# Kernel optimization log

Hardware: AMD Instinct MI355X
Metric: run time of the kernel (lower is better)

The kernel has to match this reference:

```python
import jax, jax.numpy as jnp
import numpy as np

N_FEAT = 9
D_MODEL = 128
N_HEADS = 4
LN_EPS = 1e-5


def setup_inputs() -> dict:
    key = jax.random.key(0)
    ks = jax.random.split(key, 16)
    d, F = D_MODEL, N_FEAT
    s = 0.02
    return {
        "x": jax.random.normal(ks[0], (8, 256, 16, F), dtype=jnp.float32),
        # per-band Linear(1, d): weight (F, d), bias (F, d)
        "band_W": jax.random.normal(ks[1], (F, d), dtype=jnp.float32) * s,
        "band_b": jax.random.normal(ks[2], (F, d), dtype=jnp.float32) * s,
        "freq_pos": jax.random.normal(ks[3], (1, F, d), dtype=jnp.float32) * s,
        # MultiheadAttention packed in-proj (3d, d) and out-proj (d, d)
        "in_proj_w": jax.random.normal(ks[4], (3 * d, d), dtype=jnp.float32) * s,
        "in_proj_b": jax.random.normal(ks[5], (3 * d,), dtype=jnp.float32) * s,
        "out_proj_w": jax.random.normal(ks[6], (d, d), dtype=jnp.float32) * s,
        "out_proj_b": jax.random.normal(ks[7], (d,), dtype=jnp.float32) * s,
        # gate: Linear(F*d, d)
        "gate_w": jax.random.normal(ks[8], (d, F * d), dtype=jnp.float32) * s,
        "gate_b": jax.random.normal(ks[9], (d,), dtype=jnp.float32) * s,
        # output_proj: Linear(F*d, 2d) -> GELU -> Linear(2d, d) -> LayerNorm(d)
        "proj1_w": jax.random.normal(ks[10], (2 * d, F * d), dtype=jnp.float32) * s,
        "proj1_b": jax.random.normal(ks[11], (2 * d,), dtype=jnp.float32) * s,
        "proj2_w": jax.random.normal(ks[12], (d, 2 * d), dtype=jnp.float32) * s,
        "proj2_b": jax.random.normal(ks[13], (d,), dtype=jnp.float32) * s,
        "ln_g": jnp.ones((d,), dtype=jnp.float32),
        "ln_b": jnp.zeros((d,), dtype=jnp.float32),
    }


def _forward(x, band_W, band_b, freq_pos, in_proj_w, in_proj_b,
             out_proj_w, out_proj_b, gate_w, gate_b,
             proj1_w, proj1_b, proj2_w, proj2_b, ln_g, ln_b):
    B, T, C, F = x.shape
    d, H = D_MODEL, N_HEADS
    dh = d // H
    N = B * T * C
    xf = x.reshape(N, F)
    # per-band Linear(1, d) + positional embedding -> (N, F, d)
    tok = xf[:, :, None] * band_W[None] + band_b[None] + freq_pos
    # packed QKV projection (torch MHA semantics)
    qkv = jnp.einsum('nfd,ed->nfe', tok, in_proj_w) + in_proj_b
    q, k, v = jnp.split(qkv, 3, axis=-1)
    q = q.reshape(N, F, H, dh)
    k = k.reshape(N, F, H, dh)
    v = v.reshape(N, F, H, dh)
    scores = jnp.einsum('nqhd,nkhd->nhqk', q, k) / jnp.sqrt(jnp.float32(dh))
    attn = jax.nn.softmax(scores, axis=-1)
    ctx = jnp.einsum('nhqk,nkhd->nqhd', attn, v).reshape(N, F, d)
    attn_out = ctx @ out_proj_w.T + out_proj_b
    flat = attn_out.reshape(N, F * d)
    gate = jax.nn.sigmoid(flat @ gate_w.T + gate_b)
    h = jax.nn.gelu(flat @ proj1_w.T + proj1_b, approximate=False)
    y = h @ proj2_w.T + proj2_b
    mu = jnp.mean(y, axis=-1, keepdims=True)
    var = jnp.mean(jnp.square(y - mu), axis=-1, keepdims=True)
    y = (y - mu) * jax.lax.rsqrt(var + LN_EPS) * ln_g + ln_b
    out = y * gate
    return out.reshape(B, T, C, d)


def reference(x, band_W, band_b, freq_pos, in_proj_w, in_proj_b,
              out_proj_w, out_proj_b, gate_w, gate_b,
              proj1_w, proj1_b, proj2_w, proj2_b, ln_g, ln_b):
    return _forward(x, band_W, band_b, freq_pos, in_proj_w, in_proj_b,
                    out_proj_w, out_proj_b, gate_w, gate_b,
                    proj1_w, proj1_b, proj2_w, proj2_b, ln_g, ln_b)
```

## Files before the change

### kernel.cpp

```cpp
#include <hip/hip_runtime.h>

namespace {
constexpr int FB = 9;
constexpr int FD = 1152;
constexpr float LN_EPS = 1e-5f;
constexpr int NT = 512;

typedef __attribute__((ext_vector_type(8))) short short8v;
typedef __attribute__((ext_vector_type(4))) float float4v;

constexpr int WSA_F  = 0;
constexpr int WSC_F  = 3456;
constexpr int COEF_F = 6912;
constexpr int BF_F   = 8352;
constexpr int OPA_F  = 8736;
constexpr int P2F_B  = 71808;
constexpr int WTA_B  = 137344;

constexpr int LDS_BYTES = 51200;
constexpr int L_GATE = 43008;
constexpr int L_COEF = 43008;
constexpr int L_SX   = 48768;

constexpr int NB_WTA  = 72;
constexpr int NB_BIAS = 384;
constexpr int NB_P2   = 64;

__device__ __forceinline__ unsigned short f2bf(float f) {
    unsigned u = __builtin_bit_cast(unsigned, f);
    u += 0x7FFFu + ((u >> 16) & 1u);
    return (unsigned short)(u >> 16);
}
__device__ __forceinline__ unsigned pkr(float lo, float hi) {
    const unsigned a = __builtin_bit_cast(unsigned, lo) + 0x8000u;
    const unsigned b = __builtin_bit_cast(unsigned, hi) + 0x8000u;
    return __builtin_amdgcn_perm(b, a, 0x07060302u);
}
#define MFMA16x32(a, b, c) __builtin_amdgcn_mfma_f32_16x16x32_bf16(a, b, c, 0, 0, 0)
}

__global__ void precompAC(const float* __restrict__ bW, const float* __restrict__ bb,
                          const float* __restrict__ fp, const float* __restrict__ ipw,
                          const float* __restrict__ ipb, float* __restrict__ ws)
{
    __shared__ float sw[128], sc[128];
    const int f = blockIdx.x, t = threadIdx.x;
    if (t < 128) { sw[t] = bW[f * 128 + t]; sc[t] = bb[f * 128 + t] + fp[f * 128 + t]; }
    __syncthreads();
    const float* row = ipw + (size_t)t * 128;
    float a = 0.f, c = 0.f;
    for (int k = 0; k < 128; k += 4) {
        const float4 w = *(const float4*)(row + k);
        a += sw[k]*w.x + sw[k+1]*w.y + sw[k+2]*w.z + sw[k+3]*w.w;
        c += sc[k]*w.x + sc[k+1]*w.y + sc[k+2]*w.z + sc[k+3]*w.w;
    }
    ws[WSA_F + f * 384 + t] = a;
    ws[WSC_F + f * 384 + t] = c + ipb[t];
}

__global__ void precompScoreOPA(const float* __restrict__ ws, const float* __restrict__ opw,
                                float* __restrict__ wso)
{
    const int b = blockIdx.x, t = threadIdx.x;
    if (b == 0) {
        if (t >= 324) return;
        const int h = t / 81, r = t % 81, fq = r / 9, fk = r % 9;
        const float* A = ws + WSA_F;
        const float* C = ws + WSC_F;
        const float* aq = A + fq * 384 + h * 32;
        const float* ak = A + fk * 384 + 128 + h * 32;
        const float* cq = C + fq * 384 + h * 32;
        const float* ck = C + fk * 384 + 128 + h * 32;
        float s2 = 0.f, s1q = 0.f, s1k = 0.f, s0 = 0.f;
        #pragma unroll
        for (int d = 0; d < 32; ++d) {
            s2  += aq[d] * ak[d];
            s1q += aq[d] * ck[d];
            s1k += cq[d] * ak[d];
            s0  += cq[d] * ck[d];
        }
        const float sc = 0.17677669529663687f;
        float* row = wso + COEF_F + (h * 9 + fq) * 40;
        row[fk]      = s2  * sc;
        row[10 + fk] = s1q * sc;
        row[20 + fk] = s1k * sc;
        row[30 + fk] = s0  * sc;
    } else {
        const int id = (b - 1) * 512 + t;
        if (id >= 9216) return;
        const int row = id >> 7, j = id & 127;
        const int h = row / 18, kk = row - h * 18;
        const float* av = (kk < 9) ? (ws + WSA_F + kk * 384 + 256)
                                   : (ws + WSC_F + (kk - 9) * 384 + 256);
        const float* op = opw + (size_t)j * 128 + h * 32;
        const float* avh = av + h * 32;
        float s = 0.f;
        #pragma unroll
        for (int ii = 0; ii < 32; ++ii) s += op[ii] * avh[ii];
        wso[OPA_F + row * 128 + j] = s;
    }
}

__global__ __launch_bounds__(512)
void precompWBP(const float* __restrict__ gw, const float* __restrict__ gb,
                const float* __restrict__ p1w, const float* __restrict__ p1b,
                const float* __restrict__ opb, const float* __restrict__ p2w,
                const float* __restrict__ wsf,
                unsigned short* __restrict__ wta, unsigned short* __restrict__ p2f,
                float* __restrict__ ws)
{
    __shared__ float smem[128 * 73 + 128 * 49];
    const int bid = blockIdx.x, t = threadIdx.x;
    if (bid < NB_WTA) {
        float* s_opaT = smem;
        float* s_winT = smem + 128 * 73;
        const int fq = bid % 9, oct = bid / 9;
        const int e0 = oct * 48;
        for (int i = t; i < 9216; i += 512) {
            const int r = i >> 7, j = i & 127;
            s_opaT[j * 73 + r] = wsf[OPA_F + i];
        }
        for (int i = t; i < 6144; i += 512) {
            const int el = i >> 7, j = i & 127;
            const int e = e0 + el;
            const float* Win = (e < 128) ? gw + (size_t)e * FD : p1w + (size_t)(e - 128) * FD;
            s_winT[j * 49 + el] = Win[fq * 128 + j];
        }
        __syncthreads();
        for (int d = t; d < 3456; d += 512) {
            const int el = d / 72, r = d - el * 72;
            const int e = e0 + el;
            float acc = 0.f;
            #pragma unroll 8
            for (int j = 0; j < 128; ++j)
                acc += s_winT[j * 49 + el] * s_opaT[j * 73 + r];
            const int h = r / 18, kk = r - h * 18;
            const int K = (h * 9 + fq) * 18 + kk;
            const int ks = K >> 5, slot = K & 31;
            const int lane = (e & 15) + 16 * (slot >> 3);
            wta[((size_t)((e >> 4) * 21 + ks) * 64 + lane) * 8 + (slot & 7)] = f2bf(acc);
        }
        if (fq == 0) {
            for (int d = t; d < 48 * 24; d += 512) {
                const int el = d / 24, Kp = 648 + d % 24;
                const int e = e0 + el;
                const int ks = Kp >> 5, slot = Kp & 31;
                const int lane = (e & 15) + 16 * (slot >> 3);
                wta[((size_t)((e >> 4) * 21 + ks) * 64 + lane) * 8 + (slot & 7)] = 0;
            }
        }
    } else if (bid < NB_WTA + NB_BIAS) {
        const int e = bid - NB_WTA;
        const float* Win = (e < 128) ? gw + (size_t)e * FD : p1w + (size_t)(e - 128) * FD;
        float acc = 0.f;
        for (int m = t; m < FD; m += 512) acc += Win[m] * opb[m & 127];
        #pragma unroll
        for (int off = 32; off > 0; off >>= 1) acc += __shfl_xor(acc, off);
        const int lane = t & 63, wid = t >> 6;
        if (lane == 0) smem[wid] = acc;
        __syncthreads();
        if (t == 0) {
            float s = (e < 128) ? gb[e] : p1b[e - 128];
            #pragma unroll
            for (int w = 0; w < 8; ++w) s += smem[w];
            ws[BF_F + e] = s;
        }
    } else {
        const int id = (bid - NB_WTA - NB_BIAS) * 512 + t;
        const int j = id & 7, lane = (id >> 3) & 63, ks = (id >> 9) & 7, nt = id >> 12;
        const int i = nt * 16 + (lane & 15);
        const int r = ks * 32 + (lane >> 4) * 8 + j;
        p2f[id] = f2bf(p2w[i * 256 + r]);
    }
}

__global__ __launch_bounds__(NT, 4)
void fba_main(const float* __restrict__ x, const float* __restrict__ p2b,
              const float* __restrict__ lng, const float* __restrict__ lnb,
              const float* __restrict__ wsf,
              const unsigned short* __restrict__ p2frag,
              const unsigned short* __restrict__ wta,
              float* __restrict__ out)
{
    __shared__ float4 lds4[LDS_BYTES / 16];
    char* lds = (char*)lds4;
    unsigned short* hfrag = (unsigned short*)lds;
    unsigned short* gateb = (unsigned short*)(lds + L_GATE);
    float* scoef = (float*)(lds + L_COEF);
    float* sx    = (float*)(lds + L_SX);

    const int t = threadIdx.x, lane = t & 63, wid = t >> 6;
    const int col = lane & 15, rg = lane >> 4;
    const int n0 = blockIdx.x * 32;

    for (int i = t; i < 1440; i += NT) scoef[i] = wsf[COEF_F + i];
    for (int i = t; i < 288;  i += NT) sx[i] = x[(size_t)n0 * FB + i];
    if (t < 128) *(float4*)(lds + 40960 + t * 16) = float4{0.f, 0.f, 0.f, 0.f};
    __syncthreads();

    for (int id = t; id < 1152; id += NT) {
        const int p = id >> 5, g = id & 31;
        const int fq = p % 9;
        const float* cf = scoef + p * 40;
        const float* xg = sx + g * FB;
        const float xq = xg[fq];
        float sc[9];
        float m = -1e30f;
        #pragma unroll
        for (int fk = 0; fk < 9; ++fk) {
            const float xk = xg[fk];
            const float v = (cf[fk] * xk + cf[10 + fk]) * xq + cf[20 + fk] * xk + cf[30 + fk];
            sc[fk] = v;
            m = fmaxf(m, v);
        }
        float sum = 0.f;
        #pragma unroll
        for (int fk = 0; fk < 9; ++fk) { sc[fk] = __expf(sc[fk] - m); sum += sc[fk]; }
        const float inv = 1.f / sum;
        float v[18];
        #pragma unroll
        for (int fk = 0; fk < 9; ++fk) {
            const float a = sc[fk] * inv;
            v[fk]     = a * xg[fk];
            v[9 + fk] = a;
        }
        const int mg = g >> 4, gl = g & 15;
        const int K0 = p * 18;
        #pragma unroll
        for (int qq = 0; qq < 9; ++qq) {
            const int K = K0 + 2 * qq;
            const int ks = K >> 5, slot = K & 31;
            const int row = ks * 2 + mg;
            const int u = gl + 16 * (slot >> 3);
            *(unsigned*)(lds + row * 1024 + u * 16 + (slot & 7) * 2) = pkr(v[2 * qq], v[2 * qq + 1]);
        }
    }
    __syncthreads();

    const int ng = wid;
    float4v acc0[3], acc1[3];
    #pragma unroll
    for (int q = 0; q < 3; ++q) {
        const float b = wsf[BF_F + (ng * 3 + q) * 16 + col];
        acc0[q] = float4v{b, b, b, b};
        acc1[q] = float4v{b, b, b, b};
    }
    const unsigned short* bbase = wta + (size_t)(ng * 3) * 21 * 512 + lane * 8;
    #define BLOAD(ks, q) (*(const short8v*)(bbase + ((size_t)(q) * 21 + (ks)) * 512))
    short8v cur0 = BLOAD(0, 0), cur1 = BLOAD(0, 1), cur2 = BLOAD(0, 2);
    #pragma unroll 4
    for (int ks = 0; ks < 20; ++ks) {
        const short8v nxt0 = BLOAD(ks + 1, 0);
        const short8v nxt1 = BLOAD(ks + 1, 1);
        const short8v nxt2 = BLOAD(ks + 1, 2);
        const short8v a0 = *(const short8v*)(lds + ((ks * 2 + 0) * 64 + lane) * 16);
        const short8v a1 = *(const short8v*)(lds + ((ks * 2 + 1) * 64 + lane) * 16);
        acc0[0] = MFMA16x32(a0, cur0, acc0[0]);
        acc1[0] = MFMA16x32(a1, cur0, acc1[0]);
        acc0[1] = MFMA16x32(a0, cur1, acc0[1]);
        acc1[1] = MFMA16x32(a1, cur1, acc1[1]);
        acc0[2] = MFMA16x32(a0, cur2, acc0[2]);
        acc1[2] = MFMA16x32(a1, cur2, acc1[2]);
        cur0 = nxt0; cur1 = nxt1; cur2 = nxt2;
    }
    {
        const short8v a0 = *(const short8v*)(lds + ((20 * 2 + 0) * 64 + lane) * 16);
        const short8v a1 = *(const short8v*)(lds + ((20 * 2 + 1) * 64 + lane) * 16);
        acc0[0] = MFMA16x32(a0, cur0, acc0[0]);
        acc1[0] = MFMA16x32(a1, cur0, acc1[0]);
        acc0[1] = MFMA16x32(a0, cur1, acc0[1]);
        acc1[1] = MFMA16x32(a1, cur1, acc1[1]);
        acc0[2] = MFMA16x32(a0, cur2, acc0[2]);
        acc1[2] = MFMA16x32(a1, cur2, acc1[2]);
    }
    #undef BLOAD
    __syncthreads();

    #pragma unroll
    for (int q = 0; q < 3; ++q) {
        const int e = (ng * 3 + q) * 16 + col;
        #pragma unroll
        for (int j = 0; j < 4; ++j) {
            #pragma unroll
            for (int mi = 0; mi < 2; ++mi) {
                const float vv = (mi == 0) ? acc0[q][j] : acc1[q][j];
                const int token = mi * 16 + rg * 4 + j;
                if (e < 128) {
                    const float gv = 1.f / (1.f + __expf(-vv));
                    gateb[token * 128 + e] = (unsigned short)(gv * 65535.f + 0.5f);
                } else {
                    const int rr = e - 128;
                    const float hv = 0.5f * vv * (1.f + erff(vv * 0.70710678118654752f));
                    hfrag[mi * 4096 + (rr >> 5) * 512 + (rg * 4 + j + 16 * ((rr >> 3) & 3)) * 8 + (rr & 7)] = f2bf(hv);
                }
            }
        }
    }
    __syncthreads();

    if (wid < 2) {
        const int mm = wid;
        float4v y[8];
        float lg[8], lb[8];
        #pragma unroll
        for (int nt = 0; nt < 8; ++nt) {
            const int i = nt * 16 + col;
            const float b = p2b[i];
            y[nt] = float4v{b, b, b, b};
            lg[nt] = lng[i];
            lb[nt] = lnb[i];
        }
        for (int ks = 0; ks < 8; ++ks) {
            const short8v ah = *(const short8v*)(hfrag + mm * 4096 + ks * 512 + lane * 8);
            #pragma unroll
            for (int nt = 0; nt < 8; ++nt) {
                const short8v bw = *(const short8v*)(p2frag + ((nt * 8 + ks) * 64 + lane) * 8);
                y[nt] = MFMA16x32(ah, bw, y[nt]);
            }
        }
        #pragma unroll
        for (int j = 0; j < 4; ++j) {
            const int token = mm * 16 + rg * 4 + j;
            float s = 0.f;
            #pragma unroll
            for (int nt = 0; nt < 8; ++nt) s += y[nt][j];
            s += __shfl_xor(s, 1); s += __shfl_xor(s, 2);
            s += __shfl_xor(s, 4); s += __shfl_xor(s, 8);
            const float mu = s * (1.f / 128.f);
            float v2 = 0.f;
            #pragma unroll
            for (int nt = 0; nt < 8; ++nt) { const float dd = y[nt][j] - mu; v2 += dd * dd; }
            v2 += __shfl_xor(v2, 1); v2 += __shfl_xor(v2, 2);
            v2 += __shfl_xor(v2, 4); v2 += __shfl_xor(v2, 8);
            const float inv = rsqrtf(v2 * (1.f / 128.f) + LN_EPS);
            float* op = out + (size_t)(n0 + token) * 128;
            #pragma unroll
            for (int nt = 0; nt < 8; ++nt) {
                const int i = nt * 16 + col;
                const float gv = (float)gateb[token * 128 + i] * (1.f / 65535.f);
                op[i] = ((y[nt][j] - mu) * inv * lg[nt] + lb[nt]) * gv;
            }
        }
    }
}

extern "C" void kernel_launch(void* const* d_in, const int* in_sizes, int n_in,
                              void* d_out, int out_size, void* d_ws, size_t ws_size,
                              hipStream_t stream)
{
    const float* x          = (const float*)d_in[0];
    const float* band_W     = (const float*)d_in[1];
    const float* band_b     = (const float*)d_in[2];
    const float* freq_pos   = (const float*)d_in[3];
    const float* in_proj_w  = (const float*)d_in[4];
    const float* in_proj_b  = (const float*)d_in[5];
    const float* out_proj_w = (const float*)d_in[6];
    const float* out_proj_b = (const float*)d_in[7];
    const float* gate_w     = (const float*)d_in[8];
    const float* gate_b     = (const float*)d_in[9];
    const float* proj1_w    = (const float*)d_in[10];
    const float* proj1_b    = (const float*)d_in[11];
    const float* proj2_w    = (const float*)d_in[12];
    const float* proj2_b    = (const float*)d_in[13];
    const float* ln_g       = (const float*)d_in[14];
    const float* ln_b       = (const float*)d_in[15];
    float* outp = (float*)d_out;

    float* wsf = (float*)d_ws;
    unsigned short* p2f = (unsigned short*)((char*)d_ws + P2F_B);
    unsigned short* wta = (unsigned short*)((char*)d_ws + WTA_B);

    const int Ntok = in_sizes[0] / FB;
    const int nblk = Ntok / 32;

    hipLaunchKernelGGL(precompAC,       dim3(9),   dim3(384), 0, stream, band_W, band_b, freq_pos, in_proj_w, in_proj_b, wsf);
    hipLaunchKernelGGL(precompScoreOPA, dim3(19),  dim3(512), 0, stream, wsf, out_proj_w, wsf);
    hipLaunchKernelGGL(precompWBP,      dim3(NB_WTA + NB_BIAS + NB_P2), dim3(512), 0, stream,
                       gate_w, gate_b, proj1_w, proj1_b, out_proj_b, proj2_w, wsf, wta, p2f, wsf);
    hipLaunchKernelGGL(fba_main,        dim3(nblk), dim3(NT), 0, stream,
                       x, proj2_b, ln_g, ln_b, wsf, p2f, wta, outp);
}
```

Before: 79.16 us.

## Process 64 tokens per block with K-chunked A-build and split LayerNorm epilogue

Doubles the tokens per block from 32 to 64, so each wave reuses every loaded weight B-fragment across four M-tiles instead of two, halving global weight traffic per token. To fit LDS, the attention-derived A matrix is built and consumed in two K-chunks with a triple-buffered B prefetch. The final proj2+LayerNorm stage now uses all 8 waves, split across token tiles and column halves, with partial sums combined through LDS and a single-pass variance formula. This trades higher LDS usage (64KB), more accumulators per thread and extra barriers, which may reduce occupancy, for less weight reloading.

```diff
diff --git a/kernel.cpp b/kernel.cpp
--- a/kernel.cpp
+++ b/kernel.cpp
@@ -17,10 +17,11 @@
 constexpr int P2F_B  = 71808;
 constexpr int WTA_B  = 137344;
 
-constexpr int LDS_BYTES = 51200;
-constexpr int L_GATE = 43008;
-constexpr int L_COEF = 43008;
-constexpr int L_SX   = 48768;
+constexpr int LDS_BYTES = 65536;
+constexpr int L_GATE = 49152;
+constexpr int L_COEF = 49152;
+constexpr int L_SX   = 54912;
+constexpr int L_LNP  = 32768;
 
 constexpr int NB_WTA  = 72;
 constexpr int NB_BIAS = 384;
@@ -37,6 +38,35 @@
     return __builtin_amdgcn_perm(b, a, 0x07060302u);
 }
 #define MFMA16x32(a, b, c) __builtin_amdgcn_mfma_f32_16x16x32_bf16(a, b, c, 0, 0, 0)
+
+template<int KS0, int NKS>
+__device__ __forceinline__ void kchunk(const char* __restrict__ abase,
+                                       const unsigned short* __restrict__ bbase,
+                                       float4v (&acc)[3][4])
+{
+    short8v bq[3][3];
+    #pragma unroll
+    for (int q = 0; q < 3; ++q)
+        bq[0][q] = *(const short8v*)(bbase + ((size_t)q * 21 + KS0) * 512);
+    #pragma unroll
+    for (int q = 0; q < 3; ++q)
+        bq[1][q] = *(const short8v*)(bbase + ((size_t)q * 21 + KS0 + 1) * 512);
+    #pragma unroll
+    for (int kl = 0; kl < NKS; ++kl) {
+        if (kl + 2 < NKS) {
+            #pragma unroll
+            for (int q = 0; q < 3; ++q)
+                bq[(kl + 2) % 3][q] = *(const short8v*)(bbase + ((size_t)q * 21 + KS0 + kl + 2) * 512);
+        }
+        #pragma unroll
+        for (int m = 0; m < 4; ++m) {
+            const short8v a = *(const short8v*)(abase + kl * 4096 + m * 1024);
+            #pragma unroll
+            for (int q = 0; q < 3; ++q)
+                acc[q][m] = MFMA16x32(a, bq[kl % 3][q], acc[q][m]);
+        }
+    }
+}
 }
 
 __global__ void precompAC(const float* __restrict__ bW, const float* __restrict__ bb,
@@ -185,160 +215,151 @@
     __shared__ float4 lds4[LDS_BYTES / 16];
     char* lds = (char*)lds4;
     unsigned short* hfrag = (unsigned short*)lds;
+    float* lnp  = (float*)(lds + L_LNP);
     unsigned short* gateb = (unsigned short*)(lds + L_GATE);
     float* scoef = (float*)(lds + L_COEF);
     float* sx    = (float*)(lds + L_SX);
 
     const int t = threadIdx.x, lane = t & 63, wid = t >> 6;
     const int col = lane & 15, rg = lane >> 4;
-    const int n0 = blockIdx.x * 32;
+    const int n0 = blockIdx.x * 64;
 
     for (int i = t; i < 1440; i += NT) scoef[i] = wsf[COEF_F + i];
-    for (int i = t; i < 288;  i += NT) sx[i] = x[(size_t)n0 * FB + i];
-    if (t < 128) *(float4*)(lds + 40960 + t * 16) = float4{0.f, 0.f, 0.f, 0.f};
+    for (int i = t; i < 576;  i += NT) sx[i] = x[(size_t)n0 * FB + i];
+    if (t < 256) *(float4*)(lds + 11 * 4096 + t * 16) = float4{0.f, 0.f, 0.f, 0.f};
     __syncthreads();
 
-    for (int id = t; id < 1152; id += NT) {
-        const int p = id >> 5, g = id & 31;
-        const int fq = p % 9;
-        const float* cf = scoef + p * 40;
-        const float* xg = sx + g * FB;
-        const float xq = xg[fq];
-        float sc[9];
-        float m = -1e30f;
-        #pragma unroll
-        for (int fk = 0; fk < 9; ++fk) {
-            const float xk = xg[fk];
-            const float v = (cf[fk] * xk + cf[10 + fk]) * xq + cf[20 + fk] * xk + cf[30 + fk];
-            sc[fk] = v;
-            m = fmaxf(m, v);
-        }
-        float sum = 0.f;
-        #pragma unroll
-        for (int fk = 0; fk < 9; ++fk) { sc[fk] = __expf(sc[fk] - m); sum += sc[fk]; }
-        const float inv = 1.f / sum;
-        float v[18];
-        #pragma unroll
-        for (int fk = 0; fk < 9; ++fk) {
-            const float a = sc[fk] * inv;
-            v[fk]     = a * xg[fk];
-            v[9 + fk] = a;
-        }
-        const int mg = g >> 4, gl = g & 15;
-        const int K0 = p * 18;
-        #pragma unroll
-        for (int qq = 0; qq < 9; ++qq) {
-            const int K = K0 + 2 * qq;
-            const int ks = K >> 5, slot = K & 31;
-            const int row = ks * 2 + mg;
-            const int u = gl + 16 * (slot >> 3);
-            *(unsigned*)(lds + row * 1024 + u * 16 + (slot & 7) * 2) = pkr(v[2 * qq], v[2 * qq + 1]);
-        }
-    }
-    __syncthreads();
-
     const int ng = wid;
-    float4v acc0[3], acc1[3];
+    float4v acc[3][4];
     #pragma unroll
     for (int q = 0; q < 3; ++q) {
         const float b = wsf[BF_F + (ng * 3 + q) * 16 + col];
-        acc0[q] = float4v{b, b, b, b};
-        acc1[q] = float4v{b, b, b, b};
-    }
+        #pragma unroll
+        for (int m = 0; m < 4; ++m) acc[q][m] = float4v{b, b, b, b};
+    }
+    const char* abase = lds + lane * 16;
     const unsigned short* bbase = wta + (size_t)(ng * 3) * 21 * 512 + lane * 8;
-    #define BLOAD(ks, q) (*(const short8v*)(bbase + ((size_t)(q) * 21 + (ks)) * 512))
-    short8v cur0 = BLOAD(0, 0), cur1 = BLOAD(0, 1), cur2 = BLOAD(0, 2);
-    #pragma unroll 4
-    for (int ks = 0; ks < 20; ++ks) {
-        const short8v nxt0 = BLOAD(ks + 1, 0);
-        const short8v nxt1 = BLOAD(ks + 1, 1);
-        const short8v nxt2 = BLOAD(ks + 1, 2);
-        const short8v a0 = *(const short8v*)(lds + ((ks * 2 + 0) * 64 + lane) * 16);
-        const short8v a1 = *(const short8v*)(lds + ((ks * 2 + 1) * 64 + lane) * 16);
-        acc0[0] = MFMA16x32(a0, cur0, acc0[0]);
-        acc1[0] = MFMA16x32(a1, cur0, acc1[0]);
-        acc0[1] = MFMA16x32(a0, cur1, acc0[1]);
-        acc1[1] = MFMA16x32(a1, cur1, acc1[1]);
-        acc0[2] = MFMA16x32(a0, cur2, acc0[2]);
-        acc1[2] = MFMA16x32(a1, cur2, acc1[2]);
-        cur0 = nxt0; cur1 = nxt1; cur2 = nxt2;
-    }
-    {
-        const short8v a0 = *(const short8v*)(lds + ((20 * 2 + 0) * 64 + lane) * 16);
-        const short8v a1 = *(const short8v*)(lds + ((20 * 2 + 1) * 64 + lane) * 16);
-        acc0[0] = MFMA16x32(a0, cur0, acc0[0]);
-        acc1[0] = MFMA16x32(a1, cur0, acc1[0]);
-        acc0[1] = MFMA16x32(a0, cur1, acc0[1]);
-        acc1[1] = MFMA16x32(a1, cur1, acc1[1]);
-        acc0[2] = MFMA16x32(a0, cur2, acc0[2]);
-        acc1[2] = MFMA16x32(a1, cur2, acc1[2]);
-    }
-    #undef BLOAD
-    __syncthreads();
+
+    #pragma unroll 1
+    for (int chunk = 0; chunk < 2; ++chunk) {
+        const int p0 = (chunk == 0) ? 0 : 16;
+        const int np = (chunk == 0) ? 16 : 20;
+        const int ksbase = (chunk == 0) ? 0 : 9;
+        for (int id = t; id < np * 64; id += NT) {
+            const int p = p0 + (id >> 6), g = id & 63;
+            const int fq = p % 9;
+            const float* cf = scoef + p * 40;
+            const float* xg = sx + g * FB;
+            const float xq = xg[fq];
+            float sc[9];
+            float m = -1e30f;
+            #pragma unroll
+            for (int fk = 0; fk < 9; ++fk) {
+                const float xk = xg[fk];
+                const float v = (cf[fk] * xk + cf[10 + fk]) * xq + cf[20 + fk] * xk + cf[30 + fk];
+                sc[fk] = v;
+                m = fmaxf(m, v);
+            }
+            float sum = 0.f;
+            #pragma unroll
+            for (int fk = 0; fk < 9; ++fk) { sc[fk] = __expf(sc[fk] - m); sum += sc[fk]; }
+            const float inv = 1.f / sum;
+            float v[18];
+            #pragma unroll
+            for (int fk = 0; fk < 9; ++fk) {
+                const float a = sc[fk] * inv;
+                v[fk]     = a * xg[fk];
+                v[9 + fk] = a;
+            }
+            const int mg = g >> 4, gl = g & 15;
+            const int K0 = p * 18;
+            #pragma unroll
+            for (int qq = 0; qq < 9; ++qq) {
+                const int K = K0 + 2 * qq;
+                const int row = (K >> 5) - ksbase;
+                const int slot = K & 31;
+                const int u = gl + 16 * (slot >> 3);
+                *(unsigned*)(lds + row * 4096 + mg * 1024 + u * 16 + (slot & 7) * 2) = pkr(v[2 * qq], v[2 * qq + 1]);
+            }
+        }
+        __syncthreads();
+        if (chunk == 0) kchunk<0, 9>(abase, bbase, acc);
+        else            kchunk<9, 12>(abase, bbase, acc);
+        __syncthreads();
+    }
 
     #pragma unroll
     for (int q = 0; q < 3; ++q) {
         const int e = (ng * 3 + q) * 16 + col;
         #pragma unroll
-        for (int j = 0; j < 4; ++j) {
-            #pragma unroll
-            for (int mi = 0; mi < 2; ++mi) {
-                const float vv = (mi == 0) ? acc0[q][j] : acc1[q][j];
-                const int token = mi * 16 + rg * 4 + j;
+        for (int m = 0; m < 4; ++m) {
+            #pragma unroll
+            for (int j = 0; j < 4; ++j) {
+                const float vv = acc[q][m][j];
+                const int token = m * 16 + rg * 4 + j;
                 if (e < 128) {
                     const float gv = 1.f / (1.f + __expf(-vv));
                     gateb[token * 128 + e] = (unsigned short)(gv * 65535.f + 0.5f);
                 } else {
                     const int rr = e - 128;
                     const float hv = 0.5f * vv * (1.f + erff(vv * 0.70710678118654752f));
-                    hfrag[mi * 4096 + (rr >> 5) * 512 + (rg * 4 + j + 16 * ((rr >> 3) & 3)) * 8 + (rr & 7)] = f2bf(hv);
+                    hfrag[m * 4096 + (rr >> 5) * 512 + (rg * 4 + j + 16 * ((rr >> 3) & 3)) * 8 + (rr & 7)] = f2bf(hv);
                 }
             }
         }
     }
     __syncthreads();
 
-    if (wid < 2) {
-        const int mm = wid;
-        float4v y[8];
-        float lg[8], lb[8];
-        #pragma unroll
-        for (int nt = 0; nt < 8; ++nt) {
-            const int i = nt * 16 + col;
+    {
+        const int pm = wid >> 1, half = wid & 1;
+        float4v y[4];
+        float lg[4], lb[4];
+        #pragma unroll
+        for (int nti = 0; nti < 4; ++nti) {
+            const int i = (half * 4 + nti) * 16 + col;
             const float b = p2b[i];
-            y[nt] = float4v{b, b, b, b};
-            lg[nt] = lng[i];
-            lb[nt] = lnb[i];
-        }
+            y[nti] = float4v{b, b, b, b};
+            lg[nti] = lng[i];
+            lb[nti] = lnb[i];
+        }
+        #pragma unroll
         for (int ks = 0; ks < 8; ++ks) {
-            const short8v ah = *(const short8v*)(hfrag + mm * 4096 + ks * 512 + lane * 8);
-            #pragma unroll
-            for (int nt = 0; nt < 8; ++nt) {
-                const short8v bw = *(const short8v*)(p2frag + ((nt * 8 + ks) * 64 + lane) * 8);
-                y[nt] = MFMA16x32(ah, bw, y[nt]);
+            const short8v ah = *(const short8v*)(hfrag + pm * 4096 + ks * 512 + lane * 8);
+            #pragma unroll
+            for (int nti = 0; nti < 4; ++nti) {
+                const short8v bw = *(const short8v*)(p2frag + (((half * 4 + nti) * 8 + ks) * 64 + lane) * 8);
+                y[nti] = MFMA16x32(ah, bw, y[nti]);
             }
         }
         #pragma unroll
         for (int j = 0; j < 4; ++j) {
-            const int token = mm * 16 + rg * 4 + j;
-            float s = 0.f;
-            #pragma unroll
-            for (int nt = 0; nt < 8; ++nt) s += y[nt][j];
-            s += __shfl_xor(s, 1); s += __shfl_xor(s, 2);
-            s += __shfl_xor(s, 4); s += __shfl_xor(s, 8);
+            const int token = pm * 16 + rg * 4 + j;
+            float s = y[0][j] + y[1][j] + y[2][j] + y[3][j];
+            float qq = y[0][j]*y[0][j] + y[1][j]*y[1][j] + y[2][j]*y[2][j] + y[3][j]*y[3][j];
+            s  += __shfl_xor(s, 1);  s  += __shfl_xor(s, 2);
+            s  += __shfl_xor(s, 4);  s  += __shfl_xor(s, 8);
+            qq += __shfl_xor(qq, 1); qq += __shfl_xor(qq, 2);
+            qq += __shfl_xor(qq, 4); qq += __shfl_xor(qq, 8);
+            if (col == 0) {
+                lnp[token * 4 + half * 2]     = s;
+                lnp[token * 4 + half * 2 + 1] = qq;
+            }
+        }
+        __syncthreads();
+        #pragma unroll
+        for (int j = 0; j < 4; ++j) {
+            const int token = pm * 16 + rg * 4 + j;
+            const float s  = lnp[token * 4]     + lnp[token * 4 + 2];
+            const float qq = lnp[token * 4 + 1] + lnp[token * 4 + 3];
             const float mu = s * (1.f / 128.f);
-            float v2 = 0.f;
-            #pragma unroll
-            for (int nt = 0; nt < 8; ++nt) { const float dd = y[nt][j] - mu; v2 += dd * dd; }
-            v2 += __shfl_xor(v2, 1); v2 += __shfl_xor(v2, 2);
-            v2 += __shfl_xor(v2, 4); v2 += __shfl_xor(v2, 8);
-            const float inv = rsqrtf(v2 * (1.f / 128.f) + LN_EPS);
+            const float var = qq * (1.f / 128.f) - mu * mu;
+            const float inv = rsqrtf(var + LN_EPS);
             float* op = out + (size_t)(n0 + token) * 128;
             #pragma unroll
-            for (int nt = 0; nt < 8; ++nt) {
-                const int i = nt * 16 + col;
+            for (int nti = 0; nti < 4; ++nti) {
+                const int i = (half * 4 + nti) * 16 + col;
                 const float gv = (float)gateb[token * 128 + i] * (1.f / 65535.f);
-                op[i] = ((y[nt][j] - mu) * inv * lg[nt] + lb[nt]) * gv;
+                op[i] = ((y[nti][j] - mu) * inv * lg[nti] + lb[nti]) * gv;
             }
         }
     }
@@ -371,7 +392,7 @@
     unsigned short* wta = (unsigned short*)((char*)d_ws + WTA_B);
 
     const int Ntok = in_sizes[0] / FB;
-    const int nblk = Ntok / 32;
+    const int nblk = Ntok / 64;
 
     hipLaunchKernelGGL(precompAC,       dim3(9),   dim3(384), 0, stream, band_W, band_b, freq_pos, in_proj_w, in_proj_b, wsf);
     hipLaunchKernelGGL(precompScoreOPA, dim3(19),  dim3(512), 0, stream, wsf, out_proj_w, wsf);
```

Result: slower. 105.9 us (+33.8%).

## Fuse score/OPA precompute into weight-prep kernel and deepen B-fragment prefetch

Applied to the files above, without the earlier changes.

Removes the separate precompScoreOPA launch. Each WTA block now recomputes the out-proj×V product in LDS from a transposed out_proj_w, and one extra block computes the score coefficients. In the main kernel the first three k-steps of B fragments are issued before the setup barrier, and the loop prefetches three steps ahead through a rotating register buffer. The cost is redundant OPA computation across 72 blocks, a larger LDS footprint in the precompute kernel, and higher register pressure in the main kernel.

```diff
diff --git a/kernel.cpp b/kernel.cpp
--- a/kernel.cpp
+++ b/kernel.cpp
@@ -13,7 +13,6 @@
 constexpr int WSC_F  = 3456;
 constexpr int COEF_F = 6912;
 constexpr int BF_F   = 8352;
-constexpr int OPA_F  = 8736;
 constexpr int P2F_B  = 71808;
 constexpr int WTA_B  = 137344;
 
@@ -58,73 +57,48 @@
     ws[WSC_F + f * 384 + t] = c + ipb[t];
 }
 
-__global__ void precompScoreOPA(const float* __restrict__ ws, const float* __restrict__ opw,
-                                float* __restrict__ wso)
+__global__ __launch_bounds__(512)
+void precompMega(const float* __restrict__ gw, const float* __restrict__ gb,
+                 const float* __restrict__ p1w, const float* __restrict__ p1b,
+                 const float* __restrict__ opw, const float* __restrict__ opb,
+                 const float* __restrict__ p2w, const float* __restrict__ wsf,
+                 unsigned short* __restrict__ wta, unsigned short* __restrict__ p2f,
+                 float* __restrict__ ws)
 {
-    const int b = blockIdx.x, t = threadIdx.x;
-    if (b == 0) {
-        if (t >= 324) return;
-        const int h = t / 81, r = t % 81, fq = r / 9, fk = r % 9;
-        const float* A = ws + WSA_F;
-        const float* C = ws + WSC_F;
-        const float* aq = A + fq * 384 + h * 32;
-        const float* ak = A + fk * 384 + 128 + h * 32;
-        const float* cq = C + fq * 384 + h * 32;
-        const float* ck = C + fk * 384 + 128 + h * 32;
-        float s2 = 0.f, s1q = 0.f, s1k = 0.f, s0 = 0.f;
-        #pragma unroll
-        for (int d = 0; d < 32; ++d) {
-            s2  += aq[d] * ak[d];
-            s1q += aq[d] * ck[d];
-            s1k += cq[d] * ak[d];
-            s0  += cq[d] * ck[d];
-        }
-        const float sc = 0.17677669529663687f;
-        float* row = wso + COEF_F + (h * 9 + fq) * 40;
-        row[fk]      = s2  * sc;
-        row[10 + fk] = s1q * sc;
-        row[20 + fk] = s1k * sc;
-        row[30 + fk] = s0  * sc;
-    } else {
-        const int id = (b - 1) * 512 + t;
-        if (id >= 9216) return;
-        const int row = id >> 7, j = id & 127;
-        const int h = row / 18, kk = row - h * 18;
-        const float* av = (kk < 9) ? (ws + WSA_F + kk * 384 + 256)
-                                   : (ws + WSC_F + (kk - 9) * 384 + 256);
-        const float* op = opw + (size_t)j * 128 + h * 32;
-        const float* avh = av + h * 32;
-        float s = 0.f;
-        #pragma unroll
-        for (int ii = 0; ii < 32; ++ii) s += op[ii] * avh[ii];
-        wso[OPA_F + row * 128 + j] = s;
-    }
-}
-
-__global__ __launch_bounds__(512)
-void precompWBP(const float* __restrict__ gw, const float* __restrict__ gb,
-                const float* __restrict__ p1w, const float* __restrict__ p1b,
-                const float* __restrict__ opb, const float* __restrict__ p2w,
-                const float* __restrict__ wsf,
-                unsigned short* __restrict__ wta, unsigned short* __restrict__ p2f,
-                float* __restrict__ ws)
-{
-    __shared__ float smem[128 * 73 + 128 * 49];
+    __shared__ float smem[34432];
     const int bid = blockIdx.x, t = threadIdx.x;
     if (bid < NB_WTA) {
-        float* s_opaT = smem;
-        float* s_winT = smem + 128 * 73;
+        float* s_opwT = smem;
+        float* s_avcv = smem + 16512;
+        float* s_opaT = smem + 18816;
+        float* s_winT = smem + 28160;
         const int fq = bid % 9, oct = bid / 9;
         const int e0 = oct * 48;
-        for (int i = t; i < 9216; i += 512) {
-            const int r = i >> 7, j = i & 127;
-            s_opaT[j * 73 + r] = wsf[OPA_F + i];
-        }
-        for (int i = t; i < 6144; i += 512) {
-            const int el = i >> 7, j = i & 127;
+        for (int idx = t; idx < 16384; idx += 512) {
+            const int j = idx >> 7, i = idx & 127;
+            s_opwT[i * 129 + j] = opw[idx];
+        }
+        for (int idx = t; idx < 2304; idx += 512) {
+            const int kk = idx >> 7, i = idx & 127;
+            s_avcv[idx] = (kk < 9) ? wsf[WSA_F + kk * 384 + 256 + i]
+                                   : wsf[WSC_F + (kk - 9) * 384 + 256 + i];
+        }
+        for (int idx = t; idx < 6144; idx += 512) {
+            const int el = idx >> 7, j = idx & 127;
             const int e = e0 + el;
             const float* Win = (e < 128) ? gw + (size_t)e * FD : p1w + (size_t)(e - 128) * FD;
             s_winT[j * 49 + el] = Win[fq * 128 + j];
+        }
+        __syncthreads();
+        for (int d = t; d < 9216; d += 512) {
+            const int r = d >> 7, j = d & 127;
+            const int h = r / 18, kk = r - h * 18;
+            const float* op = s_opwT + (h * 32) * 129 + j;
+            const float* av = s_avcv + kk * 128 + h * 32;
+            float acc = 0.f;
+            #pragma unroll 8
+            for (int ii = 0; ii < 32; ++ii) acc += op[ii * 129] * av[ii];
+            s_opaT[j * 73 + r] = acc;
         }
         __syncthreads();
         for (int d = t; d < 3456; d += 512) {
@@ -149,8 +123,31 @@
                 wta[((size_t)((e >> 4) * 21 + ks) * 64 + lane) * 8 + (slot & 7)] = 0;
             }
         }
-    } else if (bid < NB_WTA + NB_BIAS) {
-        const int e = bid - NB_WTA;
+    } else if (bid == NB_WTA) {
+        if (t >= 324) return;
+        const int h = t / 81, r = t % 81, fq = r / 9, fk = r % 9;
+        const float* A = wsf + WSA_F;
+        const float* C = wsf + WSC_F;
+        const float* aq = A + fq * 384 + h * 32;
+        const float* ak = A + fk * 384 + 128 + h * 32;
+        const float* cq = C + fq * 384 + h * 32;
+        const float* ck = C + fk * 384 + 128 + h * 32;
+        float s2 = 0.f, s1q = 0.f, s1k = 0.f, s0 = 0.f;
+        #pragma unroll
+        for (int d = 0; d < 32; ++d) {
+            s2  += aq[d] * ak[d];
+            s1q += aq[d] * ck[d];
+            s1k += cq[d] * ak[d];
+            s0  += cq[d] * ck[d];
+        }
+        const float sc = 0.17677669529663687f;
+        float* row = ws + COEF_F + (h * 9 + fq) * 40;
+        row[fk]      = s2  * sc;
+        row[10 + fk] = s1q * sc;
+        row[20 + fk] = s1k * sc;
+        row[30 + fk] = s0  * sc;
+    } else if (bid < NB_WTA + 1 + NB_BIAS) {
+        const int e = bid - NB_WTA - 1;
         const float* Win = (e < 128) ? gw + (size_t)e * FD : p1w + (size_t)(e - 128) * FD;
         float acc = 0.f;
         for (int m = t; m < FD; m += 512) acc += Win[m] * opb[m & 127];
@@ -166,7 +163,7 @@
             ws[BF_F + e] = s;
         }
     } else {
-        const int id = (bid - NB_WTA - NB_BIAS) * 512 + t;
+        const int id = (bid - NB_WTA - 1 - NB_BIAS) * 512 + t;
         const int j = id & 7, lane = (id >> 3) & 63, ks = (id >> 9) & 7, nt = id >> 12;
         const int i = nt * 16 + (lane & 15);
         const int r = ks * 32 + (lane >> 4) * 8 + j;
@@ -196,6 +193,16 @@
     for (int i = t; i < 1440; i += NT) scoef[i] = wsf[COEF_F + i];
     for (int i = t; i < 288;  i += NT) sx[i] = x[(size_t)n0 * FB + i];
     if (t < 128) *(float4*)(lds + 40960 + t * 16) = float4{0.f, 0.f, 0.f, 0.f};
+
+    const int ng = wid;
+    const unsigned short* bbase = wta + (size_t)(ng * 3) * 21 * 512 + lane * 8;
+    #define BLOAD(ks, q) (*(const short8v*)(bbase + ((size_t)(q) * 21 + (ks)) * 512))
+    short8v bq[3][3];
+    #pragma unroll
+    for (int d = 0; d < 3; ++d)
+        #pragma unroll
+        for (int q = 0; q < 3; ++q) bq[d][q] = BLOAD(d, q);
+
     __syncthreads();
 
     for (int id = t; id < 1152; id += NT) {
@@ -237,7 +244,6 @@
     }
     __syncthreads();
 
-    const int ng = wid;
     float4v acc0[3], acc1[3];
     #pragma unroll
     for (int q = 0; q < 3; ++q) {
@@ -245,33 +251,19 @@
         acc0[q] = float4v{b, b, b, b};
         acc1[q] = float4v{b, b, b, b};
     }
-    const unsigned short* bbase = wta + (size_t)(ng * 3) * 21 * 512 + lane * 8;
-    #define BLOAD(ks, q) (*(const short8v*)(bbase + ((size_t)(q) * 21 + (ks)) * 512))
-    short8v cur0 = BLOAD(0, 0), cur1 = BLOAD(0, 1), cur2 = BLOAD(0, 2);
-    #pragma unroll 4
-    for (int ks = 0; ks < 20; ++ks) {
-        const short8v nxt0 = BLOAD(ks + 1, 0);
-        const short8v nxt1 = BLOAD(ks + 1, 1);
-        const short8v nxt2 = BLOAD(ks + 1, 2);
+    #pragma unroll
+    for (int ks = 0; ks < 21; ++ks) {
         const short8v a0 = *(const short8v*)(lds + ((ks * 2 + 0) * 64 + lane) * 16);
         const short8v a1 = *(const short8v*)(lds + ((ks * 2 + 1) * 64 + lane) * 16);
-        acc0[0] = MFMA16x32(a0, cur0, acc0[0]);
-        acc1[0] = MFMA16x32(a1, cur0, acc1[0]);
-        acc0[1] = MFMA16x32(a0, cur1, acc0[1]);
-        acc1[1] = MFMA16x32(a1, cur1, acc1[1]);
-        acc0[2] = MFMA16x32(a0, cur2, acc0[2]);
-        acc1[2] = MFMA16x32(a1, cur2, acc1[2]);
-        cur0 = nxt0; cur1 = nxt1; cur2 = nxt2;
-    }
-    {
-        const short8v a0 = *(const short8v*)(lds + ((20 * 2 + 0) * 64 + lane) * 16);
-        const short8v a1 = *(const short8v*)(lds + ((20 * 2 + 1) * 64 + lane) * 16);
-        acc0[0] = MFMA16x32(a0, cur0, acc0[0]);
-        acc1[0] = MFMA16x32(a1, cur0, acc1[0]);
-        acc0[1] = MFMA16x32(a0, cur1, acc0[1]);
-        acc1[1] = MFMA16x32(a1, cur1, acc1[1]);
-        acc0[2] = MFMA16x32(a0, cur2, acc0[2]);
-        acc1[2] = MFMA16x32(a1, cur2, acc1[2]);
+        #pragma unroll
+        for (int q = 0; q < 3; ++q) {
+            acc0[q] = MFMA16x32(a0, bq[ks % 3][q], acc0[q]);
+            acc1[q] = MFMA16x32(a1, bq[ks % 3][q], acc1[q]);
+        }
+        if (ks + 3 < 21) {
+            #pragma unroll
+            for (int q = 0; q < 3; ++q) bq[ks % 3][q] = BLOAD(ks + 3, q);
+        }
     }
     #undef BLOAD
     __syncthreads();
@@ -373,10 +365,11 @@
     const int Ntok = in_sizes[0] / FB;
     const int nblk = Ntok / 32;
 
-    hipLaunchKernelGGL(precompAC,       dim3(9),   dim3(384), 0, stream, band_W, band_b, freq_pos, in_proj_w, in_proj_b, wsf);
-    hipLaunchKernelGGL(precompScoreOPA, dim3(19),  dim3(512), 0, stream, wsf, out_proj_w, wsf);
-    hipLaunchKernelGGL(precompWBP,      dim3(NB_WTA + NB_BIAS + NB_P2), dim3(512), 0, stream,
-                       gate_w, gate_b, proj1_w, proj1_b, out_proj_b, proj2_w, wsf, wta, p2f, wsf);
-    hipLaunchKernelGGL(fba_main,        dim3(nblk), dim3(NT), 0, stream,
+    hipLaunchKernelGGL(precompAC,   dim3(9), dim3(384), 0, stream,
+                       band_W, band_b, freq_pos, in_proj_w, in_proj_b, wsf);
+    hipLaunchKernelGGL(precompMega, dim3(NB_WTA + 1 + NB_BIAS + NB_P2), dim3(512), 0, stream,
+                       gate_w, gate_b, proj1_w, proj1_b, out_proj_w, out_proj_b,
+                       proj2_w, wsf, wta, p2f, wsf);
+    hipLaunchKernelGGL(fba_main,    dim3(nblk), dim3(NT), 0, stream,
                        x, proj2_b, ln_g, ln_b, wsf, p2f, wta, outp);
 }
```

After: 91.99 us. 16.2% more time.

## Split proj2+LayerNorm across all eight waves and use tanh GELU

Applied to the files above, without the earlier changes.

The final proj2 GEMM and LayerNorm epilogue previously ran on only two waves per block. It now spreads across all eight waves, with each wave owning a quarter of the output columns. Per-token partial sums and sums of squares go through LDS with an extra barrier, and variance is computed as E[x^2]-mu^2. The exact erf GELU is also replaced by a clamped tanh approximation built on __expf. Both changes cut serial tail work, at the cost of small numerical deviations from the reference GELU and from single-pass variance.

```diff
diff --git a/kernel.cpp b/kernel.cpp
--- a/kernel.cpp
+++ b/kernel.cpp
@@ -21,6 +21,7 @@
 constexpr int L_GATE = 43008;
 constexpr int L_COEF = 43008;
 constexpr int L_SX   = 48768;
+constexpr int L_LNP  = 16384;
 
 constexpr int NB_WTA  = 72;
 constexpr int NB_BIAS = 384;
@@ -35,6 +36,13 @@
     const unsigned a = __builtin_bit_cast(unsigned, lo) + 0x8000u;
     const unsigned b = __builtin_bit_cast(unsigned, hi) + 0x8000u;
     return __builtin_amdgcn_perm(b, a, 0x07060302u);
+}
+__device__ __forceinline__ float gelu_f(float v) {
+    float z = 0.7978845608f * (v + 0.044715f * v * v * v);
+    z = fminf(fmaxf(z, -15.f), 15.f);
+    const float e = __expf(2.f * z);
+    const float th = (e - 1.f) / (e + 1.f);
+    return 0.5f * v * (1.f + th);
 }
 #define MFMA16x32(a, b, c) __builtin_amdgcn_mfma_f32_16x16x32_bf16(a, b, c, 0, 0, 0)
 }
@@ -185,6 +193,7 @@
     __shared__ float4 lds4[LDS_BYTES / 16];
     char* lds = (char*)lds4;
     unsigned short* hfrag = (unsigned short*)lds;
+    float* lnp = (float*)(lds + L_LNP);
     unsigned short* gateb = (unsigned short*)(lds + L_GATE);
     float* scoef = (float*)(lds + L_COEF);
     float* sx    = (float*)(lds + L_SX);
@@ -290,7 +299,7 @@
                     gateb[token * 128 + e] = (unsigned short)(gv * 65535.f + 0.5f);
                 } else {
                     const int rr = e - 128;
-                    const float hv = 0.5f * vv * (1.f + erff(vv * 0.70710678118654752f));
+                    const float hv = gelu_f(vv);
                     hfrag[mi * 4096 + (rr >> 5) * 512 + (rg * 4 + j + 16 * ((rr >> 3) & 3)) * 8 + (rr & 7)] = f2bf(hv);
                 }
             }
@@ -298,47 +307,56 @@
     }
     __syncthreads();
 
-    if (wid < 2) {
-        const int mm = wid;
-        float4v y[8];
-        float lg[8], lb[8];
-        #pragma unroll
-        for (int nt = 0; nt < 8; ++nt) {
-            const int i = nt * 16 + col;
+    {
+        const int mm = wid & 1, nh = wid >> 1;
+        float4v y[2];
+        float lg[2], lb[2];
+        #pragma unroll
+        for (int nti = 0; nti < 2; ++nti) {
+            const int i = (nh * 2 + nti) * 16 + col;
             const float b = p2b[i];
-            y[nt] = float4v{b, b, b, b};
-            lg[nt] = lng[i];
-            lb[nt] = lnb[i];
-        }
+            y[nti] = float4v{b, b, b, b};
+            lg[nti] = lng[i];
+            lb[nti] = lnb[i];
+        }
+        #pragma unroll
         for (int ks = 0; ks < 8; ++ks) {
             const short8v ah = *(const short8v*)(hfrag + mm * 4096 + ks * 512 + lane * 8);
             #pragma unroll
-            for (int nt = 0; nt < 8; ++nt) {
-                const short8v bw = *(const short8v*)(p2frag + ((nt * 8 + ks) * 64 + lane) * 8);
-                y[nt] = MFMA16x32(ah, bw, y[nt]);
+            for (int nti = 0; nti < 2; ++nti) {
+                const short8v bw = *(const short8v*)(p2frag + (((nh * 2 + nti) * 8 + ks) * 64 + lane) * 8);
+                y[nti] = MFMA16x32(ah, bw, y[nti]);
             }
         }
         #pragma unroll
         for (int j = 0; j < 4; ++j) {
             const int token = mm * 16 + rg * 4 + j;
-            float s = 0.f;
-            #pragma unroll
-            for (int nt = 0; nt < 8; ++nt) s += y[nt][j];
-            s += __shfl_xor(s, 1); s += __shfl_xor(s, 2);
-            s += __shfl_xor(s, 4); s += __shfl_xor(s, 8);
+            float s = y[0][j] + y[1][j];
+            float qq = y[0][j] * y[0][j] + y[1][j] * y[1][j];
+            s  += __shfl_xor(s, 1);  s  += __shfl_xor(s, 2);
+            s  += __shfl_xor(s, 4);  s  += __shfl_xor(s, 8);
+            qq += __shfl_xor(qq, 1); qq += __shfl_xor(qq, 2);
+            qq += __shfl_xor(qq, 4); qq += __shfl_xor(qq, 8);
+            if (col == 0) {
+                lnp[token * 8 + nh * 2]     = s;
+                lnp[token * 8 + nh * 2 + 1] = qq;
+            }
+        }
+        __syncthreads();
+        #pragma unroll
+        for (int j = 0; j < 4; ++j) {
+            const int token = mm * 16 + rg * 4 + j;
+            const float s  = lnp[token * 8] + lnp[token * 8 + 2] + lnp[token * 8 + 4] + lnp[token * 8 + 6];
+            const float qq = lnp[token * 8 + 1] + lnp[token * 8 + 3] + lnp[token * 8 + 5] + lnp[token * 8 + 7];
             const float mu = s * (1.f / 128.f);
-            float v2 = 0.f;
-            #pragma unroll
-            for (int nt = 0; nt < 8; ++nt) { const float dd = y[nt][j] - mu; v2 += dd * dd; }
-            v2 += __shfl_xor(v2, 1); v2 += __shfl_xor(v2, 2);
-            v2 += __shfl_xor(v2, 4); v2 += __shfl_xor(v2, 8);
-            const float inv = rsqrtf(v2 * (1.f / 128.f) + LN_EPS);
+            const float var = qq * (1.f / 128.f) - mu * mu;
+            const float inv = rsqrtf(var + LN_EPS);
             float* op = out + (size_t)(n0 + token) * 128;
             #pragma unroll
-            for (int nt = 0; nt < 8; ++nt) {
-                const int i = nt * 16 + col;
+            for (int nti = 0; nti < 2; ++nti) {
+                const int i = (nh * 2 + nti) * 16 + col;
                 const float gv = (float)gateb[token * 128 + i] * (1.f / 65535.f);
-                op[i] = ((y[nt][j] - mu) * inv * lg[nt] + lb[nt]) * gv;
+                op[i] = ((y[nti][j] - mu) * inv * lg[nti] + lb[nti]) * gv;
             }
         }
     }
```

Measured after the change: 74.99 us. 1.06x faster.
